# Optimization experiments

Measured on AMD Instinct MI355X. Metric: run time of the kernel, lower is better.

Reference implementation:

```python
import math
import jax, jax.numpy as jnp
import numpy as np

H, PQ, PV = 12, 8, 12
C_S = 384
INF, EPS = 1e5, 1e-8
SOFTPLUS_INV_1 = 0.541324854612918


def _rand_rot(key, shape):
    """Random rotation matrices via normalized quaternions, shape + (3,3)."""
    q = jax.random.normal(key, shape + (4,))
    q = q / jnp.linalg.norm(q, axis=-1, keepdims=True)
    w, x, y, z = q[..., 0], q[..., 1], q[..., 2], q[..., 3]
    R = jnp.stack([
        1 - 2 * (y * y + z * z), 2 * (x * y - w * z), 2 * (x * z + w * y),
        2 * (x * y + w * z), 1 - 2 * (x * x + z * z), 2 * (y * z - w * x),
        2 * (x * z - w * y), 2 * (y * z + w * x), 1 - 2 * (x * x + y * y),
    ], axis=-1).reshape(shape + (3, 3))
    return R


def setup_inputs() -> dict:
    key = jax.random.key(0)
    ks = jax.random.split(key, 12)
    B, N1, N2 = 2, 2048, 512
    s1 = jax.random.normal(ks[0], (B, N1, C_S), dtype=jnp.float32)
    s2 = jax.random.normal(ks[1], (B, N2, C_S), dtype=jnp.float32)
    r1_rot = _rand_rot(ks[2], (B, N1)).astype(jnp.float32)
    r2_rot = _rand_rot(ks[3], (B, N2)).astype(jnp.float32)
    r1_trans = jax.random.normal(ks[4], (B, N1, 3), dtype=jnp.float32)
    r2_trans = jax.random.normal(ks[5], (B, N2, 3), dtype=jnp.float32)
    mask1 = jnp.ones((B, N1), dtype=jnp.float32)
    mask2 = jnp.ones((B, N2), dtype=jnp.float32)
    Wq = jax.random.normal(ks[6], (C_S, H * PQ * 3), dtype=jnp.float32) / math.sqrt(C_S)
    Wkv = jax.random.normal(ks[7], (C_S, H * (PQ + PV) * 3), dtype=jnp.float32) / math.sqrt(C_S)
    head_weights = jnp.full((H,), SOFTPLUS_INV_1, dtype=jnp.float32)
    Wout = jax.random.normal(ks[8], (H * PV * 4, C_S), dtype=jnp.float32) * 0.02
    bout = jnp.zeros((C_S,), dtype=jnp.float32)
    return {"s1": s1, "s2": s2, "r1_rot": r1_rot, "r1_trans": r1_trans,
            "r2_rot": r2_rot, "r2_trans": r2_trans, "mask1": mask1, "mask2": mask2,
            "Wq": Wq, "Wkv": Wkv, "head_weights": head_weights,
            "Wout": Wout, "bout": bout}


def reference(s1, s2, r1_rot, r1_trans, r2_rot, r2_trans, mask1, mask2,
              Wq, Wkv, head_weights, Wout, bout):
    B, N1, _ = s1.shape
    N2 = s2.shape[1]

    # query points: linear -> [B,N1,3,H,PQ] (torch split/stack layout) -> local [B,N1,H,PQ,3]
    q = jnp.moveaxis((s1 @ Wq).reshape(B, N1, 3, H, PQ), 2, -1)
    # rigid apply: R x + t (global frame)
    q = jnp.einsum('bimn,bihpn->bihpm', r1_rot, q) + r1_trans[:, :, None, None, :]

    kv = jnp.moveaxis((s2 @ Wkv).reshape(B, N2, 3, H, PQ + PV), 2, -1)
    kv = jnp.einsum('bjmn,bjhpn->bjhpm', r2_rot, kv) + r2_trans[:, :, None, None, :]
    k, v = kv[..., :PQ, :], kv[..., PQ:, :]  # [B,N2,H,PQ,3], [B,N2,H,PV,3]

    # sum_p ||q_p - k_p||^2 via norm expansion (avoids [B,N1,N2,H,PQ,3] tensor)
    qn = jnp.sum(q * q, axis=(-1, -2))                     # [B,N1,H]
    kn = jnp.sum(k * k, axis=(-1, -2))                     # [B,N2,H]
    cross = jnp.einsum('bihpc,bjhpc->bijh', q, k)          # [B,N1,N2,H]
    d2 = qn[:, :, None, :] + kn[:, None, :, :] - 2.0 * cross

    hw = jax.nn.softplus(head_weights) * math.sqrt(1.0 / (3 * (PQ * 9.0 / 2)))
    att = jnp.transpose(-0.5 * d2 * hw, (0, 3, 1, 2))      # [B,H,N1,N2]
    bias = INF * (mask1[:, :, None] * mask2[:, None, :] - 1.0)
    a = jax.nn.softmax(att + bias[:, None], axis=-1)

    o = jnp.einsum('bhij,bjhpc->bihpc', a, v)              # [B,N1,H,PV,3]
    # rigid invert_apply: R^T (x - t), back into local frame of residue i
    o_loc = jnp.einsum('bimn,bihpm->bihpn', r1_rot, o - r1_trans[:, :, None, None, :])

    dists = jnp.sqrt(jnp.sum(o_loc * o_loc, axis=-1) + EPS)   # [B,N1,H,PV]
    o_flat = o_loc.reshape(B, N1, H * PV, 3)
    feats = jnp.concatenate([o_flat[..., 0], o_flat[..., 1], o_flat[..., 2],
                             dists.reshape(B, N1, H * PV)], axis=-1)
    return feats @ Wout + bout
```

## Files before the change

kernel.cpp:

```cpp
#include <hip/hip_runtime.h>
#include <math.h>

#define B_ 2
#define N1_ 2048
#define N2_ 512
#define CS_ 384
#define H_ 12
#define PQ_ 8
#define PV_ 12
#define PKV_ 20
#define CQ_ (H_*PQ_*3)
#define CKV_ (H_*PKV_*3)
#define INF_ 100000.0f
#define HW_SCALE_ 0.09622504486493764f
#define LOG2E_ 1.4426950408889634f

typedef __attribute__((ext_vector_type(8))) short bf16x8;
typedef __attribute__((ext_vector_type(4))) float f32x4;

__device__ inline unsigned short f2bf(float x) {
  unsigned u = __float_as_uint(x);
  u += 0x7fffu + ((u >> 16) & 1u);
  return (unsigned short)(u >> 16);
}

__device__ inline bf16x8 cvt8(const float* __restrict__ p) {
  float4 a = *(const float4*)p;
  float4 b = *(const float4*)(p + 4);
  bf16x8 r;
  r[0] = (short)f2bf(a.x); r[1] = (short)f2bf(a.y);
  r[2] = (short)f2bf(a.z); r[3] = (short)f2bf(a.w);
  r[4] = (short)f2bf(b.x); r[5] = (short)f2bf(b.y);
  r[6] = (short)f2bf(b.z); r[7] = (short)f2bf(b.w);
  return r;
}

#define TQ_   108
#define TKV_  276
#define TWO_  216
#define VPAD_ 72
#define KN_   12
#define S1B_  768
#define S2B_  192
#define PREP_GRID_ (TQ_+TKV_+TWO_+VPAD_+KN_+S1B_+S2B_)
__global__ __launch_bounds__(256) void prep_kernel(
    const float* __restrict__ Wq, const float* __restrict__ Wkv,
    const float* __restrict__ Wout,
    const float* __restrict__ s1, const float* __restrict__ s2,
    unsigned short* __restrict__ wqT, unsigned short* __restrict__ wkvT,
    unsigned short* __restrict__ woutT,
    unsigned short* __restrict__ vtb, float* __restrict__ kn,
    unsigned short* __restrict__ s1b, unsigned short* __restrict__ s2b)
{
  __shared__ float lds[32][33];
  int blk = blockIdx.x, t = threadIdx.x;
  int rr0 = t >> 5, cc = t & 31;

  const float* src = nullptr; unsigned short* dst = nullptr;
  int K = 0, N = 0, k0 = 0, n0 = 0;
  if (blk < TQ_) {
    src = Wq; dst = wqT; K = 384; N = CQ_;
    k0 = (blk % 12) * 32; n0 = (blk / 12) * 32;
  } else if (blk < TQ_ + TKV_) {
    int b2 = blk - TQ_;
    src = Wkv; dst = wkvT; K = 384; N = CKV_;
    k0 = (b2 % 12) * 32; n0 = (b2 / 12) * 32;
  } else if (blk < TQ_ + TKV_ + TWO_) {
    int b3 = blk - TQ_ - TKV_;
    src = Wout; dst = woutT; K = 576; N = CS_;
    k0 = (b3 % 18) * 32; n0 = (b3 / 18) * 32;
  } else if (blk < TQ_ + TKV_ + TWO_ + VPAD_) {
    int idx = (blk - TQ_ - TKV_ - TWO_)*256 + t;
    int f = idx * 8;
    int run = f >> 9, off = f & 511;
    int bh = run / 12, cc2 = 36 + run % 12;
    uint4 z = {0u,0u,0u,0u};
    *(uint4*)(vtb + ((size_t)bh*48 + cc2)*512 + off) = z;
    return;
  } else if (blk < TQ_ + TKV_ + TWO_ + VPAD_ + KN_) {
    int idx = (blk - TQ_ - TKV_ - TWO_ - VPAD_)*256 + t;
    float4 z = {0.f,0.f,0.f,0.f};
    *(float4*)(kn + (size_t)idx*4) = z;
    return;
  } else if (blk < TQ_ + TKV_ + TWO_ + VPAD_ + KN_ + S1B_) {
    size_t idx = (size_t)(blk - TQ_ - TKV_ - TWO_ - VPAD_ - KN_)*256 + t;
    *(bf16x8*)(s1b + idx*8) = cvt8(s1 + idx*8);
    return;
  } else {
    size_t idx = (size_t)(blk - TQ_ - TKV_ - TWO_ - VPAD_ - KN_ - S1B_)*256 + t;
    *(bf16x8*)(s2b + idx*8) = cvt8(s2 + idx*8);
    return;
  }

  #pragma unroll
  for (int rr = 0; rr < 4; ++rr) {
    int r = rr0 + rr*8;
    if (n0 + cc < N) lds[r][cc] = src[(size_t)(k0 + r)*N + n0 + cc];
  }
  __syncthreads();
  #pragma unroll
  for (int rr = 0; rr < 4; ++rr) {
    int r = rr0 + rr*8;
    if (n0 + r < N) dst[(size_t)(n0 + r)*K + k0 + cc] = f2bf(lds[cc][r]);
  }
}

__global__ __launch_bounds__(256) void proj_mfma(
    const unsigned short* __restrict__ s1b, const unsigned short* __restrict__ s2b,
    const unsigned short* __restrict__ wqT, const unsigned short* __restrict__ wkvT,
    const float* __restrict__ r1_rot, const float* __restrict__ r1_trans,
    const float* __restrict__ r2_rot, const float* __restrict__ r2_trans,
    unsigned short* __restrict__ qgb, float* __restrict__ qn,
    unsigned short* __restrict__ kgb, unsigned short* __restrict__ vtb,
    float* __restrict__ kn)
{
  __shared__ float merge_s[2][64][13];
  int wave = threadIdx.x >> 6, lane = threadIdx.x & 63;
  int col = lane & 15, g = lane >> 4;
  int pr = wave >> 1, kh = wave & 1;
  int k0 = kh * 192;

  if (blockIdx.x < 768) {
    int pid = blockIdx.x*2 + pr;
    int strip = pid / 6;
    int nt = pid % 6;
    int i0 = strip * 16;

    f32x4 ax = {0.f,0.f,0.f,0.f}, ay = ax, az = ax;
    const unsigned short* arow = s1b + (size_t)(i0 + col)*CS_ + k0;
    const unsigned short* bx = wqT + (size_t)((nt     )*16 + col)*CS_ + k0;
    const unsigned short* by = wqT + (size_t)((nt +  6)*16 + col)*CS_ + k0;
    const unsigned short* bz = wqT + (size_t)((nt + 12)*16 + col)*CS_ + k0;
    #pragma unroll
    for (int k = 0; k < 192; k += 32) {
      bf16x8 a = *(const bf16x8*)(arow + k + g*8);
      ax = __builtin_amdgcn_mfma_f32_16x16x32_bf16(a, *(const bf16x8*)(bx + k + g*8), ax, 0,0,0);
      ay = __builtin_amdgcn_mfma_f32_16x16x32_bf16(a, *(const bf16x8*)(by + k + g*8), ay, 0,0,0);
      az = __builtin_amdgcn_mfma_f32_16x16x32_bf16(a, *(const bf16x8*)(bz + k + g*8), az, 0,0,0);
    }
    if (kh) {
      #pragma unroll
      for (int r = 0; r < 4; ++r) {
        merge_s[pr][lane][r]     = ax[r];
        merge_s[pr][lane][4 + r] = ay[r];
        merge_s[pr][lane][8 + r] = az[r];
      }
    }
    __syncthreads();
    if (kh) return;
    #pragma unroll
    for (int r = 0; r < 4; ++r) {
      ax[r] += merge_s[pr][lane][r];
      ay[r] += merge_s[pr][lane][4 + r];
      az[r] += merge_s[pr][lane][8 + r];
    }

    int p = nt*16 + col;
    int h = p >> 3, pq = p & 7;
    float qsum[4];
    #pragma unroll
    for (int r = 0; r < 4; ++r) {
      int row = i0 + g*4 + r;
      const float* R  = r1_rot   + (size_t)row*9;
      const float* tr = r1_trans + (size_t)row*3;
      float x = ax[r], y = ay[r], z = az[r];
      float g0 = R[0]*x + R[1]*y + R[2]*z + tr[0];
      float g1 = R[3]*x + R[4]*y + R[5]*z + tr[1];
      float g2 = R[6]*x + R[7]*y + R[8]*z + tr[2];
      int b = row >> 11, i = row & (N1_-1);
      size_t rbase = ((size_t)(b*H_ + h)*N1_ + i)*32;
      qgb[rbase + pq*3]     = f2bf(g0);
      qgb[rbase + pq*3 + 1] = f2bf(g1);
      qgb[rbase + pq*3 + 2] = f2bf(g2);
      if (pq == 7) {
        uint4 z4 = {0u,0u,0u,0u};
        *(uint4*)(qgb + rbase + 24) = z4;
      }
      qsum[r] = g0*g0 + g1*g1 + g2*g2;
    }
    #pragma unroll
    for (int r = 0; r < 4; ++r) {
      qsum[r] += __shfl_xor(qsum[r], 1);
      qsum[r] += __shfl_xor(qsum[r], 2);
      qsum[r] += __shfl_xor(qsum[r], 4);
    }
    if ((col & 7) == 0) {
      int hh = nt*2 + (col >> 3);
      #pragma unroll
      for (int r = 0; r < 4; ++r) {
        int row = i0 + g*4 + r;
        int b = row >> 11, i = row & (N1_-1);
        qn[(size_t)(b*H_ + hh)*N1_ + i] = qsum[r];
      }
    }
  } else {
    int pid = (blockIdx.x - 768)*2 + pr;
    int strip = pid / 15;
    int nt = pid % 15;
    int row0 = strip * 16;

    f32x4 ax = {0.f,0.f,0.f,0.f}, ay = ax, az = ax;
    const unsigned short* arow = s2b + (size_t)(row0 + col)*CS_ + k0;
    const unsigned short* bx = wkvT + (size_t)(nt*16       + col)*CS_ + k0;
    const unsigned short* by = wkvT + (size_t)(nt*16 + 240 + col)*CS_ + k0;
    const unsigned short* bz = wkvT + (size_t)(nt*16 + 480 + col)*CS_ + k0;
    #pragma unroll
    for (int k = 0; k < 192; k += 32) {
      bf16x8 a = *(const bf16x8*)(arow + k + g*8);
      ax = __builtin_amdgcn_mfma_f32_16x16x32_bf16(a, *(const bf16x8*)(bx + k + g*8), ax, 0,0,0);
      ay = __builtin_amdgcn_mfma_f32_16x16x32_bf16(a, *(const bf16x8*)(by + k + g*8), ay, 0,0,0);
      az = __builtin_amdgcn_mfma_f32_16x16x32_bf16(a, *(const bf16x8*)(bz + k + g*8), az, 0,0,0);
    }
    if (kh) {
      #pragma unroll
      for (int r = 0; r < 4; ++r) {
        merge_s[pr][lane][r]     = ax[r];
        merge_s[pr][lane][4 + r] = ay[r];
        merge_s[pr][lane][8 + r] = az[r];
      }
    }
    __syncthreads();
    if (kh) return;
    #pragma unroll
    for (int r = 0; r < 4; ++r) {
      ax[r] += merge_s[pr][lane][r];
      ay[r] += merge_s[pr][lane][4 + r];
      az[r] += merge_s[pr][lane][8 + r];
    }

    int p = nt*16 + col;
    int h = p / PKV_, pp = p % PKV_;
    #pragma unroll
    for (int r = 0; r < 4; ++r) {
      int row = row0 + g*4 + r;
      const float* R  = r2_rot   + (size_t)row*9;
      const float* tr = r2_trans + (size_t)row*3;
      float x = ax[r], y = ay[r], z = az[r];
      float g0 = R[0]*x + R[1]*y + R[2]*z + tr[0];
      float g1 = R[3]*x + R[4]*y + R[5]*z + tr[1];
      float g2 = R[6]*x + R[7]*y + R[8]*z + tr[2];
      int b = row >> 9, j = row & (N2_-1);
      int bh = b*H_ + h;
      if (pp < PQ_) {
        size_t base = ((size_t)bh*N2_ + j)*32 + pp*3;
        kgb[base]   = f2bf(g0);
        kgb[base+1] = f2bf(g1);
        kgb[base+2] = f2bf(g2);
        if (pp == 0) {
          uint4 z4 = {0u,0u,0u,0u};
          *(uint4*)(kgb + ((size_t)bh*N2_ + j)*32 + 24) = z4;
        }
        atomicAdd(&kn[(size_t)bh*N2_ + j], g0*g0 + g1*g1 + g2*g2);
      } else {
        int comp = (pp - PQ_)*3;
        size_t base = ((size_t)bh*48 + comp)*512 + j;
        vtb[base]        = f2bf(g0);
        vtb[base + 512]  = f2bf(g1);
        vtb[base + 1024] = f2bf(g2);
      }
    }
  }
}

#define RSTRIDE 72
#define OSTRIDE 51
#define WSLOT 3328
#define FSTRIDE 584
__global__ __launch_bounds__(768, 3) void attn_fused(
    const unsigned short* __restrict__ qgb, const float* __restrict__ qn,
    const unsigned short* __restrict__ kgb, const unsigned short* __restrict__ vtb,
    const float* __restrict__ kn, const float* __restrict__ mask1,
    const float* __restrict__ mask2, const float* __restrict__ hwts,
    const float* __restrict__ rot, const float* __restrict__ trans,
    const unsigned short* __restrict__ woutT, const float* __restrict__ bout,
    float* __restrict__ out)
{
  __shared__ __align__(16) unsigned char ovl[12*WSLOT];
  __shared__ __align__(16) unsigned short feats_s[16][FSTRIDE];
  __shared__ float l_s[12][16];

  int wave = threadIdx.x >> 6;
  int lane = threadIdx.x & 63;
  int col = lane & 15, g = lane >> 4;
  int b = blockIdx.x >> 7;
  int it = blockIdx.x & 127;
  int h = wave;
  int bh = b*H_ + h;

  unsigned short* ps = (unsigned short*)(ovl + wave*WSLOT);
  float*          os = (float*)(ovl + wave*WSLOT);

  float hw   = logf(1.0f + __expf(hwts[h])) * HW_SCALE_;
  float hwl  = hw * LOG2E_;
  float mneg = -INF_ * LOG2E_;

  bf16x8 qa = *(const bf16x8*)(qgb + (((size_t)bh*N1_ + it*16 + col)*32 + g*8));

  float ar[4], m1l[4];
  #pragma unroll
  for (int r = 0; r < 4; ++r) {
    int ig = it*16 + g*4 + r;
    ar[r]  = -0.5f*hwl * qn[(size_t)bh*N1_ + ig];
    m1l[r] = mask1[b*N1_ + ig] * (INF_*LOG2E_);
  }

  f32x4 ot[3];
  #pragma unroll
  for (int m = 0; m < 3; ++m) ot[m] = (f32x4){0.f,0.f,0.f,0.f};
  float l[4] = {0.f,0.f,0.f,0.f};

  const unsigned short* kbase = kgb + (size_t)bh*N2_*32;
  const unsigned short* vbase = vtb + (size_t)bh*48*512;
  const float* knp = kn + (size_t)bh*N2_;
  const float* m2p = mask2 + b*N2_;

  bf16x8 kbuf[4], vbuf[6];
  float knb[4], m2b[4];
  #pragma unroll
  for (int nt = 0; nt < 4; ++nt) {
    int jg = nt*16 + col;
    kbuf[nt] = *(const bf16x8*)(kbase + ((size_t)jg*32 + g*8));
    knb[nt] = knp[jg];
    m2b[nt] = m2p[jg];
  }
  #pragma unroll
  for (int ks = 0; ks < 2; ++ks)
    #pragma unroll
    for (int mtv = 0; mtv < 3; ++mtv)
      vbuf[ks*3 + mtv] = *(const bf16x8*)(vbase +
          ((size_t)(mtv*16 + col))*512 + ks*32 + g*8);

  for (int jt = 0; jt < 8; ++jt) {
    int j0 = jt*64;
    bf16x8 kNx[4], vNx[6];
    float knN[4], m2N[4];
    if (jt < 7) {
      int j1 = j0 + 64;
      #pragma unroll
      for (int nt = 0; nt < 4; ++nt) {
        int jg = j1 + nt*16 + col;
        kNx[nt] = *(const bf16x8*)(kbase + ((size_t)jg*32 + g*8));
        knN[nt] = knp[jg];
        m2N[nt] = m2p[jg];
      }
      #pragma unroll
      for (int ks = 0; ks < 2; ++ks)
        #pragma unroll
        for (int mtv = 0; mtv < 3; ++mtv)
          vNx[ks*3 + mtv] = *(const bf16x8*)(vbase +
              ((size_t)(mtv*16 + col))*512 + j1 + ks*32 + g*8);
    }

    #pragma unroll
    for (int nt = 0; nt < 4; ++nt) {
      f32x4 dotv = __builtin_amdgcn_mfma_f32_16x16x32_bf16(
          qa, kbuf[nt], (f32x4){0.f,0.f,0.f,0.f}, 0, 0, 0);
      float bc  = -0.5f*hwl*knb[nt];
      float m2c = m2b[nt];
      #pragma unroll
      for (int r = 0; r < 4; ++r) {
        float logit = fmaf(hwl, dotv[r], fmaf(m1l[r], m2c, mneg) + (ar[r] + bc));
        float w = __builtin_amdgcn_exp2f(logit);
        l[r] += w;
        ps[(g*4 + r)*RSTRIDE + nt*16 + col] = f2bf(w);
      }
    }
    __builtin_amdgcn_s_setprio(1);
    #pragma unroll
    for (int ks = 0; ks < 2; ++ks) {
      bf16x8 pb = *(const bf16x8*)&ps[col*RSTRIDE + ks*32 + g*8];
      #pragma unroll
      for (int mtv = 0; mtv < 3; ++mtv)
        ot[mtv] = __builtin_amdgcn_mfma_f32_16x16x32_bf16(vbuf[ks*3 + mtv], pb, ot[mtv], 0, 0, 0);
    }
    __builtin_amdgcn_s_setprio(0);

    if (jt < 7) {
      #pragma unroll
      for (int i = 0; i < 4; ++i) { kbuf[i] = kNx[i]; knb[i] = knN[i]; m2b[i] = m2N[i]; }
      #pragma unroll
      for (int i = 0; i < 6; ++i) vbuf[i] = vNx[i];
    }
  }

  #pragma unroll
  for (int r = 0; r < 4; ++r) {
    l[r] += __shfl_xor(l[r], 1);
    l[r] += __shfl_xor(l[r], 2);
    l[r] += __shfl_xor(l[r], 4);
    l[r] += __shfl_xor(l[r], 8);
  }
  __builtin_amdgcn_sched_barrier(0);
  if (col == 0) {
    #pragma unroll
    for (int r = 0; r < 4; ++r) l_s[wave][g*4 + r] = l[r];
  }
  #pragma unroll
  for (int mtv = 0; mtv < 3; ++mtv)
    #pragma unroll
    for (int r = 0; r < 4; ++r)
      os[col*OSTRIDE + mtv*16 + g*4 + r] = ot[mtv][r];
  __syncthreads();

  {
    float inv = 1.0f / l_s[wave][col];
    int ig = it*16 + col;
    int row = b*N1_ + ig;
    const float* R  = rot   + (size_t)row*9;
    const float* tr = trans + (size_t)row*3;
    float R00=R[0],R01=R[1],R02=R[2],R10=R[3],R11=R[4],R12=R[5],R20=R[6],R21=R[7],R22=R[8];
    float t0=tr[0], t1=tr[1], t2=tr[2];
    int h12 = h*PV_;
    #pragma unroll
    for (int p = 0; p < 3; ++p) {
      int pt = g*3 + p;
      float ox = os[col*OSTRIDE + pt*3+0]*inv - t0;
      float oy = os[col*OSTRIDE + pt*3+1]*inv - t1;
      float oz = os[col*OSTRIDE + pt*3+2]*inv - t2;
      float lx = R00*ox + R10*oy + R20*oz;
      float ly = R01*ox + R11*oy + R21*oz;
      float lz = R02*ox + R12*oy + R22*oz;
      float dist = sqrtf(lx*lx + ly*ly + lz*lz + 1e-8f);
      feats_s[col][      h12 + pt] = f2bf(lx);
      feats_s[col][144 + h12 + pt] = f2bf(ly);
      feats_s[col][288 + h12 + pt] = f2bf(lz);
      feats_s[col][432 + h12 + pt] = f2bf(dist);
    }
  }
  __syncthreads();

  {
    int n0 = wave * 32;
    f32x4 acc0 = {0.f,0.f,0.f,0.f}, acc1 = acc0;
    const unsigned short* b0 = woutT + (size_t)(n0      + col)*576;
    const unsigned short* b1 = woutT + (size_t)(n0 + 16 + col)*576;
    #pragma unroll 3
    for (int k = 0; k < 576; k += 32) {
      bf16x8 a = *(const bf16x8*)&feats_s[col][k + g*8];
      acc0 = __builtin_amdgcn_mfma_f32_16x16x32_bf16(a, *(const bf16x8*)(b0 + k + g*8), acc0, 0,0,0);
      acc1 = __builtin_amdgcn_mfma_f32_16x16x32_bf16(a, *(const bf16x8*)(b1 + k + g*8), acc1, 0,0,0);
    }
    int rowbase = b*N1_ + it*16;
    float bb0 = bout[n0 + col];
    float bb1 = bout[n0 + 16 + col];
    #pragma unroll
    for (int r = 0; r < 4; ++r) {
      size_t orow = (size_t)(rowbase + g*4 + r)*CS_;
      out[orow + n0 + col]      = acc0[r] + bb0;
      out[orow + n0 + 16 + col] = acc1[r] + bb1;
    }
  }
}

extern "C" void kernel_launch(void* const* d_in, const int* in_sizes, int n_in,
                              void* d_out, int out_size, void* d_ws, size_t ws_size,
                              hipStream_t stream) {
  const float* s1       = (const float*)d_in[0];
  const float* s2       = (const float*)d_in[1];
  const float* r1_rot   = (const float*)d_in[2];
  const float* r1_trans = (const float*)d_in[3];
  const float* r2_rot   = (const float*)d_in[4];
  const float* r2_trans = (const float*)d_in[5];
  const float* mask1    = (const float*)d_in[6];
  const float* mask2    = (const float*)d_in[7];
  const float* Wq       = (const float*)d_in[8];
  const float* Wkv      = (const float*)d_in[9];
  const float* hwts     = (const float*)d_in[10];
  const float* Wout     = (const float*)d_in[11];
  const float* bout     = (const float*)d_in[12];
  float* out = (float*)d_out;

  float* qn = (float*)d_ws;
  float* kn = qn + (size_t)B_*H_*N1_;
  unsigned short* qgb  = (unsigned short*)(kn + (size_t)B_*H_*N2_);
  unsigned short* kgb  = qgb  + (size_t)B_*H_*N1_*32;
  unsigned short* vtb  = kgb  + (size_t)B_*H_*N2_*32;
  unsigned short* wqT  = vtb  + (size_t)B_*H_*48*512;
  unsigned short* wkvT = wqT  + (size_t)CQ_*CS_;
  unsigned short* woutT= wkvT + (size_t)CKV_*CS_;
  unsigned short* s1b  = woutT+ (size_t)CS_*576;
  unsigned short* s2b  = s1b  + (size_t)B_*N1_*CS_;

  prep_kernel<<<PREP_GRID_, 256, 0, stream>>>(
      Wq, Wkv, Wout, s1, s2, wqT, wkvT, woutT, vtb, kn, s1b, s2b);
  proj_mfma<<<1248, 256, 0, stream>>>(s1b, s2b, wqT, wkvT, r1_rot, r1_trans,
                                      r2_rot, r2_trans, qgb, qn, kgb, vtb, kn);
  attn_fused<<<B_*(N1_/16), 768, 0, stream>>>(qgb, qn, kgb, vtb, kn, mask1, mask2,
                                              hwts, r1_rot, r1_trans, woutT, bout, out);
}
```

Measured before the change: 145.8 us.

## Fuse query projection and rigid transform into attention kernel

After: 150.1 us. 1.03x slower.

```diff
diff --git a/kernel.cpp b/kernel.cpp
--- a/kernel.cpp
+++ b/kernel.cpp
@@ -106,11 +106,9 @@
 }
 
 __global__ __launch_bounds__(256) void proj_mfma(
-    const unsigned short* __restrict__ s1b, const unsigned short* __restrict__ s2b,
-    const unsigned short* __restrict__ wqT, const unsigned short* __restrict__ wkvT,
-    const float* __restrict__ r1_rot, const float* __restrict__ r1_trans,
+    const unsigned short* __restrict__ s2b,
+    const unsigned short* __restrict__ wkvT,
     const float* __restrict__ r2_rot, const float* __restrict__ r2_trans,
-    unsigned short* __restrict__ qgb, float* __restrict__ qn,
     unsigned short* __restrict__ kgb, unsigned short* __restrict__ vtb,
     float* __restrict__ kn)
 {
@@ -120,144 +118,69 @@
   int pr = wave >> 1, kh = wave & 1;
   int k0 = kh * 192;
 
-  if (blockIdx.x < 768) {
-    int pid = blockIdx.x*2 + pr;
-    int strip = pid / 6;
-    int nt = pid % 6;
-    int i0 = strip * 16;
-
-    f32x4 ax = {0.f,0.f,0.f,0.f}, ay = ax, az = ax;
-    const unsigned short* arow = s1b + (size_t)(i0 + col)*CS_ + k0;
-    const unsigned short* bx = wqT + (size_t)((nt     )*16 + col)*CS_ + k0;
-    const unsigned short* by = wqT + (size_t)((nt +  6)*16 + col)*CS_ + k0;
-    const unsigned short* bz = wqT + (size_t)((nt + 12)*16 + col)*CS_ + k0;
-    #pragma unroll
-    for (int k = 0; k < 192; k += 32) {
-      bf16x8 a = *(const bf16x8*)(arow + k + g*8);
-      ax = __builtin_amdgcn_mfma_f32_16x16x32_bf16(a, *(const bf16x8*)(bx + k + g*8), ax, 0,0,0);
-      ay = __builtin_amdgcn_mfma_f32_16x16x32_bf16(a, *(const bf16x8*)(by + k + g*8), ay, 0,0,0);
-      az = __builtin_amdgcn_mfma_f32_16x16x32_bf16(a, *(const bf16x8*)(bz + k + g*8), az, 0,0,0);
-    }
-    if (kh) {
-      #pragma unroll
-      for (int r = 0; r < 4; ++r) {
-        merge_s[pr][lane][r]     = ax[r];
-        merge_s[pr][lane][4 + r] = ay[r];
-        merge_s[pr][lane][8 + r] = az[r];
-      }
-    }
-    __syncthreads();
-    if (kh) return;
+  int pid = blockIdx.x*2 + pr;
+  int strip = pid / 15;
+  int nt = pid % 15;
+  int row0 = strip * 16;
+
+  f32x4 ax = {0.f,0.f,0.f,0.f}, ay = ax, az = ax;
+  const unsigned short* arow = s2b + (size_t)(row0 + col)*CS_ + k0;
+  const unsigned short* bx = wkvT + (size_t)(nt*16       + col)*CS_ + k0;
+  const unsigned short* by = wkvT + (size_t)(nt*16 + 240 + col)*CS_ + k0;
+  const unsigned short* bz = wkvT + (size_t)(nt*16 + 480 + col)*CS_ + k0;
+  #pragma unroll
+  for (int k = 0; k < 192; k += 32) {
+    bf16x8 a = *(const bf16x8*)(arow + k + g*8);
+    ax = __builtin_amdgcn_mfma_f32_16x16x32_bf16(a, *(const bf16x8*)(bx + k + g*8), ax, 0,0,0);
+    ay = __builtin_amdgcn_mfma_f32_16x16x32_bf16(a, *(const bf16x8*)(by + k + g*8), ay, 0,0,0);
+    az = __builtin_amdgcn_mfma_f32_16x16x32_bf16(a, *(const bf16x8*)(bz + k + g*8), az, 0,0,0);
+  }
+  if (kh) {
     #pragma unroll
     for (int r = 0; r < 4; ++r) {
-      ax[r] += merge_s[pr][lane][r];
-      ay[r] += merge_s[pr][lane][4 + r];
-      az[r] += merge_s[pr][lane][8 + r];
-    }
-
-    int p = nt*16 + col;
-    int h = p >> 3, pq = p & 7;
-    float qsum[4];
-    #pragma unroll
-    for (int r = 0; r < 4; ++r) {
-      int row = i0 + g*4 + r;
-      const float* R  = r1_rot   + (size_t)row*9;
-      const float* tr = r1_trans + (size_t)row*3;
-      float x = ax[r], y = ay[r], z = az[r];
-      float g0 = R[0]*x + R[1]*y + R[2]*z + tr[0];
-      float g1 = R[3]*x + R[4]*y + R[5]*z + tr[1];
-      float g2 = R[6]*x + R[7]*y + R[8]*z + tr[2];
-      int b = row >> 11, i = row & (N1_-1);
-      size_t rbase = ((size_t)(b*H_ + h)*N1_ + i)*32;
-      qgb[rbase + pq*3]     = f2bf(g0);
-      qgb[rbase + pq*3 + 1] = f2bf(g1);
-      qgb[rbase + pq*3 + 2] = f2bf(g2);
-      if (pq == 7) {
+      merge_s[pr][lane][r]     = ax[r];
+      merge_s[pr][lane][4 + r] = ay[r];
+      merge_s[pr][lane][8 + r] = az[r];
+    }
+  }
+  __syncthreads();
+  if (kh) return;
+  #pragma unroll
+  for (int r = 0; r < 4; ++r) {
+    ax[r] += merge_s[pr][lane][r];
+    ay[r] += merge_s[pr][lane][4 + r];
+    az[r] += merge_s[pr][lane][8 + r];
+  }
+
+  int p = nt*16 + col;
+  int h = p / PKV_, pp = p % PKV_;
+  #pragma unroll
+  for (int r = 0; r < 4; ++r) {
+    int row = row0 + g*4 + r;
+    const float* R  = r2_rot   + (size_t)row*9;
+    const float* tr = r2_trans + (size_t)row*3;
+    float x = ax[r], y = ay[r], z = az[r];
+    float g0 = R[0]*x + R[1]*y + R[2]*z + tr[0];
+    float g1 = R[3]*x + R[4]*y + R[5]*z + tr[1];
+    float g2 = R[6]*x + R[7]*y + R[8]*z + tr[2];
+    int b = row >> 9, j = row & (N2_-1);
+    int bh = b*H_ + h;
+    if (pp < PQ_) {
+      size_t base = ((size_t)bh*N2_ + j)*32 + pp*3;
+      kgb[base]   = f2bf(g0);
+      kgb[base+1] = f2bf(g1);
+      kgb[base+2] = f2bf(g2);
+      if (pp == 0) {
         uint4 z4 = {0u,0u,0u,0u};
-        *(uint4*)(qgb + rbase + 24) = z4;
-      }
-      qsum[r] = g0*g0 + g1*g1 + g2*g2;
-    }
-    #pragma unroll
-    for (int r = 0; r < 4; ++r) {
-      qsum[r] += __shfl_xor(qsum[r], 1);
-      qsum[r] += __shfl_xor(qsum[r], 2);
-      qsum[r] += __shfl_xor(qsum[r], 4);
-    }
-    if ((col & 7) == 0) {
-      int hh = nt*2 + (col >> 3);
-      #pragma unroll
-      for (int r = 0; r < 4; ++r) {
-        int row = i0 + g*4 + r;
-        int b = row >> 11, i = row & (N1_-1);
-        qn[(size_t)(b*H_ + hh)*N1_ + i] = qsum[r];
-      }
-    }
-  } else {
-    int pid = (blockIdx.x - 768)*2 + pr;
-    int strip = pid / 15;
-    int nt = pid % 15;
-    int row0 = strip * 16;
-
-    f32x4 ax = {0.f,0.f,0.f,0.f}, ay = ax, az = ax;
-    const unsigned short* arow = s2b + (size_t)(row0 + col)*CS_ + k0;
-    const unsigned short* bx = wkvT + (size_t)(nt*16       + col)*CS_ + k0;
-    const unsigned short* by = wkvT + (size_t)(nt*16 + 240 + col)*CS_ + k0;
-    const unsigned short* bz = wkvT + (size_t)(nt*16 + 480 + col)*CS_ + k0;
-    #pragma unroll
-    for (int k = 0; k < 192; k += 32) {
-      bf16x8 a = *(const bf16x8*)(arow + k + g*8);
-      ax = __builtin_amdgcn_mfma_f32_16x16x32_bf16(a, *(const bf16x8*)(bx + k + g*8), ax, 0,0,0);
-      ay = __builtin_amdgcn_mfma_f32_16x16x32_bf16(a, *(const bf16x8*)(by + k + g*8), ay, 0,0,0);
-      az = __builtin_amdgcn_mfma_f32_16x16x32_bf16(a, *(const bf16x8*)(bz + k + g*8), az, 0,0,0);
-    }
-    if (kh) {
-      #pragma unroll
-      for (int r = 0; r < 4; ++r) {
-        merge_s[pr][lane][r]     = ax[r];
-        merge_s[pr][lane][4 + r] = ay[r];
-        merge_s[pr][lane][8 + r] = az[r];
-      }
-    }
-    __syncthreads();
-    if (kh) return;
-    #pragma unroll
-    for (int r = 0; r < 4; ++r) {
-      ax[r] += merge_s[pr][lane][r];
-      ay[r] += merge_s[pr][lane][4 + r];
-      az[r] += merge_s[pr][lane][8 + r];
-    }
-
-    int p = nt*16 + col;
-    int h = p / PKV_, pp = p % PKV_;
-    #pragma unroll
-    for (int r = 0; r < 4; ++r) {
-      int row = row0 + g*4 + r;
-      const float* R  = r2_rot   + (size_t)row*9;
-      const float* tr = r2_trans + (size_t)row*3;
-      float x = ax[r], y = ay[r], z = az[r];
-      float g0 = R[0]*x + R[1]*y + R[2]*z + tr[0];
-      float g1 = R[3]*x + R[4]*y + R[5]*z + tr[1];
-      float g2 = R[6]*x + R[7]*y + R[8]*z + tr[2];
-      int b = row >> 9, j = row & (N2_-1);
-      int bh = b*H_ + h;
-      if (pp < PQ_) {
-        size_t base = ((size_t)bh*N2_ + j)*32 + pp*3;
-        kgb[base]   = f2bf(g0);
-        kgb[base+1] = f2bf(g1);
-        kgb[base+2] = f2bf(g2);
-        if (pp == 0) {
-          uint4 z4 = {0u,0u,0u,0u};
-          *(uint4*)(kgb + ((size_t)bh*N2_ + j)*32 + 24) = z4;
-        }
-        atomicAdd(&kn[(size_t)bh*N2_ + j], g0*g0 + g1*g1 + g2*g2);
-      } else {
-        int comp = (pp - PQ_)*3;
-        size_t base = ((size_t)bh*48 + comp)*512 + j;
-        vtb[base]        = f2bf(g0);
-        vtb[base + 512]  = f2bf(g1);
-        vtb[base + 1024] = f2bf(g2);
-      }
+        *(uint4*)(kgb + ((size_t)bh*N2_ + j)*32 + 24) = z4;
+      }
+      atomicAdd(&kn[(size_t)bh*N2_ + j], g0*g0 + g1*g1 + g2*g2);
+    } else {
+      int comp = (pp - PQ_)*3;
+      size_t base = ((size_t)bh*48 + comp)*512 + j;
+      vtb[base]        = f2bf(g0);
+      vtb[base + 512]  = f2bf(g1);
+      vtb[base + 1024] = f2bf(g2);
     }
   }
 }
@@ -267,7 +190,7 @@
 #define WSLOT 3328
 #define FSTRIDE 584
 __global__ __launch_bounds__(768, 3) void attn_fused(
-    const unsigned short* __restrict__ qgb, const float* __restrict__ qn,
+    const unsigned short* __restrict__ s1b, const unsigned short* __restrict__ wqT,
     const unsigned short* __restrict__ kgb, const unsigned short* __restrict__ vtb,
     const float* __restrict__ kn, const float* __restrict__ mask1,
     const float* __restrict__ mask2, const float* __restrict__ hwts,
@@ -289,20 +212,72 @@
 
   unsigned short* ps = (unsigned short*)(ovl + wave*WSLOT);
   float*          os = (float*)(ovl + wave*WSLOT);
+  unsigned short* qpad  = (unsigned short*)(ovl + wave*WSLOT);
+  float*          qnpad = (float*)(ovl + wave*WSLOT + 1024);
 
   float hw   = logf(1.0f + __expf(hwts[h])) * HW_SCALE_;
   float hwl  = hw * LOG2E_;
   float mneg = -INF_ * LOG2E_;
 
-  bf16x8 qa = *(const bf16x8*)(qgb + (((size_t)bh*N1_ + it*16 + col)*32 + g*8));
+  {
+    f32x4 acc0 = {0.f,0.f,0.f,0.f}, acc1 = acc0;
+    const unsigned short* arow = s1b + (size_t)(b*N1_ + it*16 + col)*CS_;
+    int brow1 = h*8 + (col & 7) + (col >> 3)*96;
+    int brow2 = 192 + h*8 + (col & 7);
+    const unsigned short* bp1 = wqT + (size_t)brow1*CS_;
+    const unsigned short* bp2 = wqT + (size_t)brow2*CS_;
+    #pragma unroll
+    for (int k = 0; k < CS_; k += 32) {
+      bf16x8 a = *(const bf16x8*)(arow + k + g*8);
+      acc0 = __builtin_amdgcn_mfma_f32_16x16x32_bf16(a, *(const bf16x8*)(bp1 + k + g*8), acc0, 0,0,0);
+      acc1 = __builtin_amdgcn_mfma_f32_16x16x32_bf16(a, *(const bf16x8*)(bp2 + k + g*8), acc1, 0,0,0);
+    }
+    float c1v[4];
+    #pragma unroll
+    for (int r = 0; r < 4; ++r) c1v[r] = __shfl_xor(acc0[r], 8);
+    *(unsigned*)((char*)qpad + col*64 + 48 + g*4) = 0u;
+    if (col < 8) {
+      int p = col;
+      float qsum[4];
+      #pragma unroll
+      for (int r = 0; r < 4; ++r) {
+        int il = g*4 + r;
+        int row = b*N1_ + it*16 + il;
+        const float* R  = rot   + (size_t)row*9;
+        const float* tr = trans + (size_t)row*3;
+        float x = acc0[r], y = c1v[r], z = acc1[r];
+        float g0 = R[0]*x + R[1]*y + R[2]*z + tr[0];
+        float g1 = R[3]*x + R[4]*y + R[5]*z + tr[1];
+        float g2 = R[6]*x + R[7]*y + R[8]*z + tr[2];
+        qpad[il*32 + p*3    ] = f2bf(g0);
+        qpad[il*32 + p*3 + 1] = f2bf(g1);
+        qpad[il*32 + p*3 + 2] = f2bf(g2);
+        qsum[r] = g0*g0 + g1*g1 + g2*g2;
+      }
+      #pragma unroll
+      for (int r = 0; r < 4; ++r) {
+        qsum[r] += __shfl_xor(qsum[r], 1);
+        qsum[r] += __shfl_xor(qsum[r], 2);
+        qsum[r] += __shfl_xor(qsum[r], 4);
+      }
+      if (col == 0) {
+        #pragma unroll
+        for (int r = 0; r < 4; ++r) qnpad[g*4 + r] = qsum[r];
+      }
+    }
+  }
+  __builtin_amdgcn_sched_barrier(0);
+
+  bf16x8 qa = *(const bf16x8*)(qpad + col*32 + g*8);
 
   float ar[4], m1l[4];
   #pragma unroll
   for (int r = 0; r < 4; ++r) {
     int ig = it*16 + g*4 + r;
-    ar[r]  = -0.5f*hwl * qn[(size_t)bh*N1_ + ig];
+    ar[r]  = -0.5f*hwl * qnpad[g*4 + r];
     m1l[r] = mask1[b*N1_ + ig] * (INF_*LOG2E_);
   }
+  __builtin_amdgcn_sched_barrier(0);
 
   f32x4 ot[3];
   #pragma unroll
@@ -470,10 +445,8 @@
   const float* bout     = (const float*)d_in[12];
   float* out = (float*)d_out;
 
-  float* qn = (float*)d_ws;
-  float* kn = qn + (size_t)B_*H_*N1_;
-  unsigned short* qgb  = (unsigned short*)(kn + (size_t)B_*H_*N2_);
-  unsigned short* kgb  = qgb  + (size_t)B_*H_*N1_*32;
+  float* kn = (float*)d_ws;
+  unsigned short* kgb  = (unsigned short*)(kn + (size_t)B_*H_*N2_);
   unsigned short* vtb  = kgb  + (size_t)B_*H_*N2_*32;
   unsigned short* wqT  = vtb  + (size_t)B_*H_*48*512;
   unsigned short* wkvT = wqT  + (size_t)CQ_*CS_;
@@ -483,8 +456,7 @@
 
   prep_kernel<<<PREP_GRID_, 256, 0, stream>>>(
       Wq, Wkv, Wout, s1, s2, wqT, wkvT, woutT, vtb, kn, s1b, s2b);
-  proj_mfma<<<1248, 256, 0, stream>>>(s1b, s2b, wqT, wkvT, r1_rot, r1_trans,
-                                      r2_rot, r2_trans, qgb, qn, kgb, vtb, kn);
-  attn_fused<<<B_*(N1_/16), 768, 0, stream>>>(qgb, qn, kgb, vtb, kn, mask1, mask2,
+  proj_mfma<<<480, 256, 0, stream>>>(s2b, wkvT, r2_rot, r2_trans, kgb, vtb, kn);
+  attn_fused<<<B_*(N1_/16), 768, 0, stream>>>(s1b, wqT, kgb, vtb, kn, mask1, mask2,
                                               hwts, r1_rot, r1_trans, woutT, bout, out);
 }
```
